# Kernel optimization log

Hardware: AMD Instinct MI355X
Metric: run time of the kernel (lower is better)

The kernel has to match this reference:

```python
import jax, jax.numpy as jnp
import numpy as np

D_STATE = 8
DT_RANK = 16
D_CONV = 4


def layernorm(x, w, b, eps=1e-5):
    mu = jnp.mean(x, axis=-1, keepdims=True)
    var = jnp.var(x, axis=-1, keepdims=True)
    return (x - mu) * jax.lax.rsqrt(var + eps) * w + b


def silu(x):
    return x * jax.nn.sigmoid(x)


def dwconv_causal(x, w, b):
    # x: [B,L,D], w: [D,K] depthwise causal conv (mamba conv1d, padding=K-1 then truncate)
    K = w.shape[1]
    xp = jnp.pad(x, ((0, 0), (K - 1, 0), (0, 0)))
    y = jax.lax.conv_general_dilated(
        xp, w.T[:, None, :], (1,), 'VALID',
        dimension_numbers=('NWC', 'WIO', 'NWC'),
        feature_group_count=w.shape[0])
    return y + b


def selective_scan(u, dt, A, Bm, Cm, Dp):
    # u, dt: [b,l,d]; A: [d,n]; Bm, Cm: [b,l,n]; Dp: [d]
    def step(h, inp):
        dt_t, B_t, C_t, u_t = inp           # [b,d],[b,n],[b,n],[b,d]
        dA = jnp.exp(dt_t[..., None] * A)   # [b,d,n]
        h = dA * h + dt_t[..., None] * B_t[:, None, :] * u_t[..., None]
        y = jnp.einsum('bdn,bn->bd', h, C_t)
        return h, y
    b, l, d = u.shape
    h0 = jnp.zeros((b, d, A.shape[1]), u.dtype)
    xs = (dt.transpose(1, 0, 2), Bm.transpose(1, 0, 2),
          Cm.transpose(1, 0, 2), u.transpose(1, 0, 2))
    _, ys = jax.lax.scan(step, h0, xs)
    return ys.transpose(1, 0, 2) + u * Dp


def scan_dir(x, xe, cw, cb, cew, ceb, xpw, dtw, dtb, A_log, Dp):
    # one scan direction: u from x (input0 path), dt/B/C from xe (extra_emb path)
    xc = silu(dwconv_causal(x, cw, cb))
    ec = silu(dwconv_causal(xe, cew, ceb))
    dbl = ec @ xpw.T                                   # [b,l,dt_rank+2n]
    dtr = dbl[..., :DT_RANK]
    Bm = dbl[..., DT_RANK:DT_RANK + D_STATE]
    Cm = dbl[..., DT_RANK + D_STATE:]
    dt = jax.nn.softplus(dtr @ dtw.T + dtb)
    A = -jnp.exp(A_log)
    return selective_scan(xc, dt, A, Bm, Cm, Dp)


def forward(input0, input1, norm0_w, norm0_b, norm1_w, norm1_b,
            in_proj_w, in_proj_extra_w,
            convx_w, convx_b, conve_w, conve_b,
            convx_w_r, convx_b_r, conve_w_r, conve_b_r,
            xproj_w, xproj_w_r, dtproj_w, dtproj_b, dtproj_w_r, dtproj_b_r,
            A_log, A_log_r, Dp, Dp_r, outnorm_w, outnorm_b, outproj_w):
    skip = input0
    h0 = layernorm(input0, norm0_w, norm0_b)
    h1 = layernorm(input1, norm1_w, norm1_b)
    xz = h0 @ in_proj_w.T                     # [b,l,2d]
    d = in_proj_w.shape[0] // 2
    x, z = xz[..., :d], xz[..., d:]
    xe = h1 @ in_proj_extra_w.T               # [b,l,d]
    # forward-direction scan
    y_f = scan_dir(x, xe, convx_w, convx_b, conve_w, conve_b,
                   xproj_w, dtproj_w, dtproj_b, A_log, Dp)
    # backward-direction scan (flip sequence, scan, flip back)
    xr, xer = jnp.flip(x, 1), jnp.flip(xe, 1)
    y_b = scan_dir(xr, xer, convx_w_r, convx_b_r, conve_w_r, conve_b_r,
                   xproj_w_r, dtproj_w_r, dtproj_b_r, A_log_r, Dp_r)
    y = (y_f + jnp.flip(y_b, 1)) * 0.5        # if_devide_out=True
    y = layernorm(y, outnorm_w, outnorm_b)    # use_norm=True
    y = y * silu(z)
    out = y @ outproj_w.T
    return out + skip


def setup_inputs() -> dict:
    key = jax.random.key(0)
    B, H, W, dim = 2, 128, 128, 256
    L, d, n, dtr, K = H * W, dim, D_STATE, DT_RANK, D_CONV
    ks = jax.random.split(key, 24)
    s = 0.02
    inp = {
        'input0': jax.random.normal(ks[0], (B, L, dim), jnp.float32),
        'input1': jax.random.normal(ks[1], (B, L, dim), jnp.float32),
        'norm0_w': jnp.ones((dim,), jnp.float32),
        'norm0_b': jnp.zeros((dim,), jnp.float32),
        'norm1_w': jnp.ones((dim,), jnp.float32),
        'norm1_b': jnp.zeros((dim,), jnp.float32),
        'in_proj_w': jax.random.normal(ks[2], (2 * d, dim), jnp.float32) * s,
        'in_proj_extra_w': jax.random.normal(ks[3], (d, dim), jnp.float32) * s,
        'convx_w': jax.random.normal(ks[4], (d, K), jnp.float32) * 0.2,
        'convx_b': jnp.zeros((d,), jnp.float32),
        'conve_w': jax.random.normal(ks[5], (d, K), jnp.float32) * 0.2,
        'conve_b': jnp.zeros((d,), jnp.float32),
        'convx_w_r': jax.random.normal(ks[6], (d, K), jnp.float32) * 0.2,
        'convx_b_r': jnp.zeros((d,), jnp.float32),
        'conve_w_r': jax.random.normal(ks[7], (d, K), jnp.float32) * 0.2,
        'conve_b_r': jnp.zeros((d,), jnp.float32),
        'xproj_w': jax.random.normal(ks[8], (dtr + 2 * n, d), jnp.float32) * s,
        'xproj_w_r': jax.random.normal(ks[9], (dtr + 2 * n, d), jnp.float32) * s,
        'dtproj_w': jax.random.normal(ks[10], (d, dtr), jnp.float32) * 0.1,
        'dtproj_b': jax.random.uniform(ks[11], (d,), jnp.float32, -4.0, -2.0),
        'dtproj_w_r': jax.random.normal(ks[12], (d, dtr), jnp.float32) * 0.1,
        'dtproj_b_r': jax.random.uniform(ks[13], (d,), jnp.float32, -4.0, -2.0),
        'A_log': jnp.tile(jnp.log(jnp.arange(1, n + 1, dtype=jnp.float32)), (d, 1)),
        'A_log_r': jnp.tile(jnp.log(jnp.arange(1, n + 1, dtype=jnp.float32)), (d, 1)),
        'Dp': jnp.ones((d,), jnp.float32),
        'Dp_r': jnp.ones((d,), jnp.float32),
        'outnorm_w': jnp.ones((d,), jnp.float32),
        'outnorm_b': jnp.zeros((d,), jnp.float32),
        'outproj_w': jax.random.normal(ks[14], (dim, d), jnp.float32) * s,
    }
    return inp


def reference(input0, input1, norm0_w, norm0_b, norm1_w, norm1_b,
              in_proj_w, in_proj_extra_w,
              convx_w, convx_b, conve_w, conve_b,
              convx_w_r, convx_b_r, conve_w_r, conve_b_r,
              xproj_w, xproj_w_r, dtproj_w, dtproj_b, dtproj_w_r, dtproj_b_r,
              A_log, A_log_r, Dp, Dp_r, outnorm_w, outnorm_b, outproj_w):
    return forward(input0, input1, norm0_w, norm0_b, norm1_w, norm1_b,
                   in_proj_w, in_proj_extra_w,
                   convx_w, convx_b, conve_w, conve_b,
                   convx_w_r, convx_b_r, conve_w_r, conve_b_r,
                   xproj_w, xproj_w_r, dtproj_w, dtproj_b, dtproj_w_r, dtproj_b_r,
                   A_log, A_log_r, Dp, Dp_r, outnorm_w, outnorm_b, outproj_w)
```

## Files before the change

### kernel.cpp

```cpp
#include <hip/hip_runtime.h>
#include <math.h>

#define L_SEQ 16384
#define DIM 256
#define NST 8
#define RNK 16
#define S_TOT 32768
#define NCH 512
#define CLH 32

typedef __attribute__((ext_vector_type(8))) short bf16x8;
typedef __attribute__((ext_vector_type(4))) float f32x4;

__device__ __forceinline__ float bf2f(unsigned short u) {
  union { unsigned int i; float f; } v; v.i = ((unsigned int)u) << 16; return v.f;
}
__device__ __forceinline__ unsigned short f2bf(float x) {
  union { float f; unsigned int i; } v; v.f = x;
  unsigned int r = v.i + 0x7fffu + ((v.i >> 16) & 1u);
  return (unsigned short)(r >> 16);
}
__device__ __forceinline__ float rcpf(float x) {
  return __builtin_amdgcn_rcpf(x);
}

__global__ __launch_bounds__(256) void wconv(
    const float* __restrict__ w0, const float* __restrict__ w1,
    const float* __restrict__ w2, unsigned short* __restrict__ out) {
  int i = blockIdx.x * 256 + threadIdx.x;
  if (i < 131072) out[i] = f2bf(w0[i]);
  else if (i < 196608) out[i] = f2bf(w1[i - 131072]);
  else out[i] = f2bf(w2[i - 196608]);
}

__global__ __launch_bounds__(256) void ln_norm(
    const float* __restrict__ in0, const float* __restrict__ in1,
    const float* __restrict__ w0, const float* __restrict__ b0,
    const float* __restrict__ w1, const float* __restrict__ b1,
    unsigned short* __restrict__ h0, unsigned short* __restrict__ h1) {
  int which = blockIdx.y;
  int row = blockIdx.x * 4 + (threadIdx.x >> 6);
  int lane = threadIdx.x & 63;
  const float* x = (which ? in1 : in0) + (size_t)row * DIM;
  const float* w = which ? w1 : w0;
  const float* b = which ? b1 : b0;
  unsigned short* h = which ? h1 : h0;
  float4 v = *(const float4*)&x[lane * 4];
  float s = v.x + v.y + v.z + v.w;
  float s2 = v.x * v.x + v.y * v.y + v.z * v.z + v.w * v.w;
  for (int off = 32; off; off >>= 1) {
    s += __shfl_xor(s, off);
    s2 += __shfl_xor(s2, off);
  }
  float mean = s * (1.0f / DIM);
  float var = s2 * (1.0f / DIM) - mean * mean;
  float rstd = rsqrtf(var + 1e-5f);
  float4 wv = *(const float4*)&w[lane * 4];
  float4 bv = *(const float4*)&b[lane * 4];
  ushort4 out;
  out.x = f2bf((v.x - mean) * rstd * wv.x + bv.x);
  out.y = f2bf((v.y - mean) * rstd * wv.y + bv.y);
  out.z = f2bf((v.z - mean) * rstd * wv.z + bv.z);
  out.w = f2bf((v.w - mean) * rstd * wv.w + bv.w);
  *(ushort4*)&h[(size_t)row * DIM + lane * 4] = out;
}

template <int BF16C, int ADDIN>
__global__ __launch_bounds__(256) void gemm64(
    const unsigned short* __restrict__ A, int lda,
    const unsigned short* __restrict__ Wb,
    void* __restrict__ Cv, const float* __restrict__ addp, int Nn) {
  __shared__ unsigned short As[64 * 256];
  __shared__ unsigned short Ws[64 * 256];
  int tid = threadIdx.x;
  int n0 = blockIdx.x * 64, m0 = blockIdx.y * 64;
  for (int i = 0; i < 8; ++i) {
    int f8 = tid + i * 256;
    int r = f8 >> 5, c8 = (f8 & 31) * 8;
    int sc = c8 ^ ((r & 7) << 3);
    *(uint4*)&As[r * 256 + sc] = *(const uint4*)&A[(size_t)(m0 + r) * lda + c8];
    *(uint4*)&Ws[r * 256 + sc] = *(const uint4*)&Wb[(size_t)(n0 + r) * 256 + c8];
  }
  __syncthreads();
  int wid = tid >> 6, lane = tid & 63;
  int wm = wid >> 1, wn = wid & 1;
  int l15 = lane & 15, lk = (lane >> 4) * 8;
  f32x4 acc[2][2] = {};
  for (int ks = 0; ks < 8; ++ks) {
    int kcol = ks * 32 + lk;
    bf16x8 af[2], bf_[2];
    for (int mf = 0; mf < 2; ++mf) {
      int row = wm * 32 + mf * 16 + l15;
      af[mf] = *(const bf16x8*)&As[row * 256 + (kcol ^ ((row & 7) << 3))];
    }
    for (int nf = 0; nf < 2; ++nf) {
      int row = wn * 32 + nf * 16 + l15;
      bf_[nf] = *(const bf16x8*)&Ws[row * 256 + (kcol ^ ((row & 7) << 3))];
    }
    for (int mf = 0; mf < 2; ++mf)
      for (int nf = 0; nf < 2; ++nf)
        acc[mf][nf] = __builtin_amdgcn_mfma_f32_16x16x32_bf16(
            af[mf], bf_[nf], acc[mf][nf], 0, 0, 0);
  }
  for (int mf = 0; mf < 2; ++mf)
    for (int nf = 0; nf < 2; ++nf) {
      int row = m0 + wm * 32 + mf * 16 + (lane >> 4) * 4;
      int col = n0 + wn * 32 + nf * 16 + l15;
      for (int v = 0; v < 4; ++v) {
        size_t off = (size_t)(row + v) * Nn + col;
        float val = acc[mf][nf][v];
        if (ADDIN) val += addp[off];
        if (BF16C) ((unsigned short*)Cv)[off] = f2bf(val);
        else       ((float*)Cv)[off] = val;
      }
    }
}

__global__ __launch_bounds__(256) void xproj_mfma(
    const unsigned short* __restrict__ xe,
    const float* __restrict__ conve_w, const float* __restrict__ conve_b,
    const float* __restrict__ conve_w_r, const float* __restrict__ conve_b_r,
    const float* __restrict__ xproj_w, const float* __restrict__ xproj_w_r,
    float* __restrict__ dbl2) {
  __shared__ unsigned short ecS[64 * 256];
  __shared__ unsigned short xwS[32 * 256];
  int chunk = blockIdx.x;
  int dir = blockIdx.y;
  int b = chunk >> 8;
  int t0 = (chunk & 255) * 64;
  int tid = threadIdx.x;
  const float* cw = dir ? conve_w_r : conve_w;
  const float* cb = dir ? conve_b_r : conve_b;
  const float* xw = dir ? xproj_w_r : xproj_w;

  for (int i = tid; i < 32 * 256; i += 256) {
    int o = i >> 8, dd = i & 255;
    xwS[o * 256 + (((dd & ~7) ^ ((o & 7) << 3)) | (dd & 7))] = f2bf(xw[i]);
  }

  {
    int c = tid;
    float w0 = cw[c * 4 + 0], w1 = cw[c * 4 + 1], w2 = cw[c * 4 + 2],
          w3 = cw[c * 4 + 3], bias = cb[c];
    size_t bL = (size_t)b * L_SEQ;
    auto loadx = [&](int t) -> float {
      if (t < 0) return 0.f;
      int src = dir ? (L_SEQ - 1 - t) : t;
      return bf2f(xe[(bL + src) * DIM + c]);
    };
    float xm3 = loadx(t0 - 3), xm2 = loadx(t0 - 2), xm1 = loadx(t0 - 1);
    const unsigned short* xp =
        &xe[(bL + (dir ? (L_SEQ - 1 - t0) : t0)) * DIM + c];
    int xstep = dir ? -DIM : DIM;
    int cbase = c & ~7, clow = c & 7;
    for (int tl = 0; tl < 64; ++tl) {
      float xin = bf2f(*xp); xp += xstep;
      float pre = w0 * xm3 + w1 * xm2 + w2 * xm1 + w3 * xin + bias;
      float u = pre * rcpf(1.f + __expf(-pre));
      xm3 = xm2; xm2 = xm1; xm1 = xin;
      ecS[tl * 256 + ((cbase ^ ((tl & 7) << 3)) | clow)] = f2bf(u);
    }
  }
  __syncthreads();

  int wid = tid >> 6, lane = tid & 63;
  int l15 = lane & 15, lk = (lane >> 4) * 8;
  f32x4 acc[2] = {};
  for (int kk = 0; kk < 8; ++kk) {
    int kcol = kk * 32 + lk;
    int row = wid * 16 + l15;
    bf16x8 af = *(const bf16x8*)&ecS[row * 256 + (kcol ^ ((row & 7) << 3))];
    for (int ni = 0; ni < 2; ++ni) {
      int o = ni * 16 + l15;
      bf16x8 bfr = *(const bf16x8*)&xwS[o * 256 + (kcol ^ ((o & 7) << 3))];
      acc[ni] = __builtin_amdgcn_mfma_f32_16x16x32_bf16(af, bfr, acc[ni], 0, 0, 0);
    }
  }
  size_t mbase = (size_t)dir * S_TOT + (size_t)chunk * 64;
  int rloc = wid * 16 + (lane >> 4) * 4;
  for (int ni = 0; ni < 2; ++ni) {
    int o = ni * 16 + l15;
    for (int v = 0; v < 4; ++v)
      dbl2[(mbase + rloc + v) * 32 + o] = acc[ni][v];
  }
}

__global__ __launch_bounds__(256) void dt_mfma(
    const float* __restrict__ dbl2,
    const float* __restrict__ dtw, const float* __restrict__ dtw_r,
    const float* __restrict__ dtb, const float* __restrict__ dtb_r,
    unsigned short* __restrict__ dt_arr) {
  __shared__ unsigned short dtwS[256 * 32];
  __shared__ unsigned short dtrS[64 * 32];
  __shared__ unsigned short outS[64 * 256];
  int m0 = blockIdx.x * 64;
  int dir = (blockIdx.x >= 512) ? 1 : 0;
  int tid = threadIdx.x;
  const float* dw = dir ? dtw_r : dtw;
  const float* db = dir ? dtb_r : dtb;
  {
    uint4 z; z.x = 0; z.y = 0; z.z = 0; z.w = 0;
    for (int i = tid; i < 1280; i += 256) {
      if (i < 1024) ((uint4*)dtwS)[i] = z;
      else          ((uint4*)dtrS)[i - 1024] = z;
    }
  }
  __syncthreads();
  for (int it = 0; it < 4; ++it) {
    int idx = tid + it * 256;
    int c = idx >> 2, k4 = idx & 3;
    float4 v = *(const float4*)&dw[c * 16 + k4 * 4];
    uint2 pk;
    pk.x = (unsigned int)f2bf(v.x) | ((unsigned int)f2bf(v.y) << 16);
    pk.y = (unsigned int)f2bf(v.z) | ((unsigned int)f2bf(v.w) << 16);
    int byte = c * 64 + (((k4 >> 1) ^ (c & 3)) << 4) + ((k4 & 1) << 3);
    *(uint2*)((char*)dtwS + byte) = pk;
  }
  {
    int r = tid >> 2, k4 = tid & 3;
    float4 v = *(const float4*)&dbl2[(size_t)(m0 + r) * 32 + k4 * 4];
    uint2 pk;
    pk.x = (unsigned int)f2bf(v.x) | ((unsigned int)f2bf(v.y) << 16);
    pk.y = (unsigned int)f2bf(v.z) | ((unsigned int)f2bf(v.w) << 16);
    int byte = r * 64 + (((k4 >> 1) ^ (r & 3)) << 4) + ((k4 & 1) << 3);
    *(uint2*)((char*)dtrS + byte) = pk;
  }
  __syncthreads();
  int wid = tid >> 6, lane = tid & 63;
  int l15 = lane & 15, lkc = lane >> 4;
  bf16x8 af[4];
  for (int mi = 0; mi < 4; ++mi) {
    int r = mi * 16 + l15;
    af[mi] = *(const bf16x8*)((char*)dtrS + r * 64 + ((lkc ^ (r & 3)) << 4));
  }
  f32x4 acc[4][4] = {};
  for (int ni = 0; ni < 4; ++ni) {
    int c = (wid * 4 + ni) * 16 + l15;
    bf16x8 bfr = *(const bf16x8*)((char*)dtwS + c * 64 + ((lkc ^ (c & 3)) << 4));
    for (int mi = 0; mi < 4; ++mi)
      acc[mi][ni] = __builtin_amdgcn_mfma_f32_16x16x32_bf16(
          af[mi], bfr, acc[mi][ni], 0, 0, 0);
  }
  for (int ni = 0; ni < 4; ++ni) {
    int c = (wid * 4 + ni) * 16 + l15;
    float bias_ = db[c];
    int cb_ = c & ~7, cl_ = c & 7;
    for (int mi = 0; mi < 4; ++mi) {
      int rb = mi * 16 + (lane >> 4) * 4;
      for (int v = 0; v < 4; ++v) {
        int r = rb + v;
        float xdt = acc[mi][ni][v] + bias_;
        float dtv = (xdt > 15.f) ? xdt : __logf(1.f + __expf(xdt));
        outS[r * 256 + ((cb_ ^ ((r & 7) << 3)) | cl_)] = f2bf(dtv);
      }
    }
  }
  __syncthreads();
  for (int it = 0; it < 8; ++it) {
    int i = tid + it * 256;
    int r = i >> 5, cg = (i & 31) * 8;
    uint4 val = *(const uint4*)&outS[r * 256 + (cg ^ ((r & 7) << 3))];
    *(uint4*)&dt_arr[(size_t)(m0 + r) * 256 + cg] = val;
  }
}

__global__ __launch_bounds__(256) void u_compute(
    const unsigned short* __restrict__ xz,
    const float* __restrict__ convx_w, const float* __restrict__ convx_b,
    const float* __restrict__ convx_w_r, const float* __restrict__ convx_b_r,
    unsigned short* __restrict__ u_arr) {
  int chunk = blockIdx.x;
  int dir = blockIdx.y;
  int b = chunk >> 9;
  int t0 = (chunk & 511) * 32;
  int c = threadIdx.x;
  const float* cw = dir ? convx_w_r : convx_w;
  const float* cb = dir ? convx_b_r : convx_b;
  float w0 = cw[c * 4 + 0], w1 = cw[c * 4 + 1], w2 = cw[c * 4 + 2],
        w3 = cw[c * 4 + 3], bias = cb[c];
  size_t dtbase = (size_t)dir * S_TOT + (size_t)b * L_SEQ;
  size_t bL = (size_t)b * L_SEQ;
  float xm3, xm2, xm1;
  {
    auto loadx = [&](int t) -> float {
      if (t < 0) return 0.f;
      int src = dir ? (L_SEQ - 1 - t) : t;
      return bf2f(xz[(bL + src) * 512 + c]);
    };
    xm3 = loadx(t0 - 3); xm2 = loadx(t0 - 2); xm1 = loadx(t0 - 1);
  }
  const unsigned short* xp = &xz[(bL + (dir ? (L_SEQ - 1 - t0) : t0)) * 512 + c];
  int xstep = dir ? -512 : 512;
  unsigned short* op = &u_arr[(dtbase + t0) * DIM + c];
  for (int tl = 0; tl < 32; ++tl) {
    float xin = bf2f(*xp); xp += xstep;
    float pre = w0 * xm3 + w1 * xm2 + w2 * xm1 + w3 * xin + bias;
    float u = pre * rcpf(1.f + __expf(-pre));
    xm3 = xm2; xm2 = xm1; xm1 = xin;
    *op = f2bf(u); op += DIM;
  }
}

#define DA8(FASTA)                                                    \
  float dA[NST];                                                      \
  if (FASTA) {                                                        \
    float e1 = __expf(-dtv);                                          \
    dA[0] = e1;                                                       \
    for (int n = 1; n < NST; ++n) dA[n] = dA[n - 1] * e1;             \
  } else {                                                            \
    for (int n = 0; n < NST; ++n) dA[n] = __expf(dtv * Ar[n]);        \
  }

template <int USE_UDT>
__global__ __launch_bounds__(256) void scan_pass1(
    const unsigned short* __restrict__ xz, const float* __restrict__ dbl2,
    const unsigned short* __restrict__ u_arr,
    const unsigned short* __restrict__ dt_arr,
    const float* __restrict__ convx_w, const float* __restrict__ convx_b,
    const float* __restrict__ convx_w_r, const float* __restrict__ convx_b_r,
    const float* __restrict__ dtproj_w, const float* __restrict__ dtproj_b,
    const float* __restrict__ dtproj_w_r, const float* __restrict__ dtproj_b_r,
    const float* __restrict__ A_log, const float* __restrict__ A_log_r,
    float* __restrict__ Pc, float* __restrict__ Qc) {
  int chunk = blockIdx.x, b = blockIdx.y, dir = blockIdx.z;
  int d = threadIdx.x;
  const float* al = dir ? A_log_r : A_log;
  float w0 = 0.f, w1 = 0.f, w2 = 0.f, w3 = 0.f, bias = 0.f, dbias = 0.f;
  float dwreg[RNK];
  if (!USE_UDT) {
    const float* cw = dir ? convx_w_r : convx_w;
    const float* cb = dir ? convx_b_r : convx_b;
    const float* dw = dir ? dtproj_w_r : dtproj_w;
    const float* dbp = dir ? dtproj_b_r : dtproj_b;
    w0 = cw[d * 4 + 0]; w1 = cw[d * 4 + 1]; w2 = cw[d * 4 + 2];
    w3 = cw[d * 4 + 3]; bias = cb[d]; dbias = dbp[d];
    for (int r = 0; r < RNK; ++r) dwreg[r] = dw[d * RNK + r];
  }
  float Ar[NST];
  bool fa = true;
  for (int n = 0; n < NST; ++n) {
    Ar[n] = -__expf(al[d * NST + n]);
    fa = fa && (fabsf(Ar[n] + (float)(n + 1)) < 1e-4f * (float)(n + 1));
  }
  bool fastA = (__ballot(fa) == ~0ULL);

  __shared__ float dblS[CLH][32];
  int t0 = chunk * CLH;
  size_t dtbase = (size_t)dir * S_TOT + (size_t)b * L_SEQ;
  if (USE_UDT) {
    int i = d;
    dblS[i >> 3][i & 7] = dbl2[(dtbase + t0 + (i >> 3)) * 32 + 16 + (i & 7)];
  } else {
    for (int i = d; i < CLH * 32; i += 256)
      dblS[i >> 5][i & 31] = dbl2[(dtbase + t0) * 32 + i];
  }
  __syncthreads();
  auto loadx = [&](int t) -> float {
    if (t < 0) return 0.f;
    int srct = dir ? (L_SEQ - 1 - t) : t;
    return bf2f(xz[((size_t)b * L_SEQ + srct) * 512 + d]);
  };
  float xm3 = 0.f, xm2 = 0.f, xm1 = 0.f;
  if (!USE_UDT) { xm3 = loadx(t0 - 3); xm2 = loadx(t0 - 2); xm1 = loadx(t0 - 1); }
  const unsigned short* up = &u_arr[(dtbase + t0) * DIM + d];
  const unsigned short* dtp = &dt_arr[(dtbase + t0) * DIM + d];
  float Q[NST];
  for (int n = 0; n < NST; ++n) Q[n] = 0.f;
  float sdt = 0.f;
  const int BOFF = USE_UDT ? 0 : 16;

#define P1_STEP(FASTA)                                                     \
  {                                                                        \
    const float* row = dblS[tl];                                           \
    float u, dtv;                                                          \
    if (USE_UDT) {                                                         \
      u = bf2f(*up); up += DIM;                                            \
      dtv = bf2f(*dtp); dtp += DIM;                                        \
    } else {                                                               \
      float xin = loadx(t0 + tl);                                          \
      float pre = w0 * xm3 + w1 * xm2 + w2 * xm1 + w3 * xin + bias;        \
      u = pre * rcpf(1.f + __expf(-pre));                                  \
      xm3 = xm2; xm2 = xm1; xm1 = xin;                                     \
      float4 q0 = *(const float4*)(row);                                   \
      float4 q1 = *(const float4*)(row + 4);                               \
      float4 q2 = *(const float4*)(row + 8);                               \
      float4 q3 = *(const float4*)(row + 12);                              \
      float xdt = dbias + q0.x * dwreg[0] + q0.y * dwreg[1] +              \
                  q0.z * dwreg[2] + q0.w * dwreg[3] + q1.x * dwreg[4] +    \
                  q1.y * dwreg[5] + q1.z * dwreg[6] + q1.w * dwreg[7] +    \
                  q2.x * dwreg[8] + q2.y * dwreg[9] + q2.z * dwreg[10] +   \
                  q2.w * dwreg[11] + q3.x * dwreg[12] + q3.y * dwreg[13] + \
                  q3.z * dwreg[14] + q3.w * dwreg[15];                     \
      dtv = (xdt > 15.f) ? xdt : __logf(1.f + __expf(xdt));                \
    }                                                                      \
    float du = dtv * u;                                                    \
    sdt += dtv;                                                            \
    DA8(FASTA)                                                             \
    float4 B0 = *(const float4*)(row + BOFF);                              \
    float4 B1 = *(const float4*)(row + BOFF + 4);                          \
    Q[0] = dA[0] * Q[0] + du * B0.x; Q[1] = dA[1] * Q[1] + du * B0.y;      \
    Q[2] = dA[2] * Q[2] + du * B0.z; Q[3] = dA[3] * Q[3] + du * B0.w;      \
    Q[4] = dA[4] * Q[4] + du * B1.x; Q[5] = dA[5] * Q[5] + du * B1.y;      \
    Q[6] = dA[6] * Q[6] + du * B1.z; Q[7] = dA[7] * Q[7] + du * B1.w;      \
  }

  if (fastA) {
    for (int tl = 0; tl < CLH; ++tl) P1_STEP(1)
  } else {
    for (int tl = 0; tl < CLH; ++tl) P1_STEP(0)
  }
#undef P1_STEP

  float P[NST];
  if (fastA) {
    float E = __expf(-sdt);
    P[0] = E;
    for (int n = 1; n < NST; ++n) P[n] = P[n - 1] * E;
  } else {
    for (int n = 0; n < NST; ++n) P[n] = __expf(Ar[n] * sdt);
  }
  size_t obase = ((((size_t)(dir * 2 + b)) * NCH + chunk) * DIM + d) * NST;
  for (int n = 0; n < NST; ++n) { Pc[obase + n] = P[n]; Qc[obase + n] = Q[n]; }
}

__global__ __launch_bounds__(256) void scan_mid(
    float* __restrict__ Pc, const float* __restrict__ Qc) {
  int idx = blockIdx.x * 256 + threadIdx.x;
  int dn = idx & 2047;
  int db_ = idx >> 11;
  size_t base = (size_t)db_ * NCH * 2048 + dn;
  float h = 0.f;
  for (int c0 = 0; c0 < NCH; c0 += 8) {
    size_t off = base + (size_t)c0 * 2048;
    float P[8], Q[8];
#pragma unroll
    for (int j = 0; j < 8; ++j) {
      P[j] = Pc[off + (size_t)j * 2048];
      Q[j] = Qc[off + (size_t)j * 2048];
    }
#pragma unroll
    for (int j = 0; j < 8; ++j) {
      Pc[off + (size_t)j * 2048] = h;
      h = P[j] * h + Q[j];
    }
  }
}

template <int MODE>
__global__ __launch_bounds__(256) void scan_pass2(
    const unsigned short* __restrict__ xz, const float* __restrict__ dbl2,
    unsigned short* __restrict__ u_arr,
    const unsigned short* __restrict__ dt_arr,
    const float* __restrict__ convx_w, const float* __restrict__ convx_b,
    const float* __restrict__ convx_w_r, const float* __restrict__ convx_b_r,
    const float* __restrict__ dtproj_w, const float* __restrict__ dtproj_b,
    const float* __restrict__ dtproj_w_r, const float* __restrict__ dtproj_b_r,
    const float* __restrict__ A_log, const float* __restrict__ A_log_r,
    const float* __restrict__ Dp, const float* __restrict__ Dp_r,
    const float* __restrict__ Hinit, unsigned short* __restrict__ ycomb,
    int dirParam) {
  int chunk = blockIdx.x, b = blockIdx.y;
  int dir = MODE ? blockIdx.z : dirParam;
  int d = threadIdx.x;
  const float* al = dir ? A_log_r : A_log;
  float Dv = (dir ? Dp_r : Dp)[d];
  float w0 = 0.f, w1 = 0.f, w2 = 0.f, w3 = 0.f, bias = 0.f, dbias = 0.f;
  float dwreg[RNK];
  if (!MODE) {
    const float* cw = dir ? convx_w_r : convx_w;
    const float* cb = dir ? convx_b_r : convx_b;
    const float* dw = dir ? dtproj_w_r : dtproj_w;
    const float* dbp = dir ? dtproj_b_r : dtproj_b;
    w0 = cw[d * 4 + 0]; w1 = cw[d * 4 + 1]; w2 = cw[d * 4 + 2];
    w3 = cw[d * 4 + 3]; bias = cb[d];
    dbias = dbp[d];
    for (int r = 0; r < RNK; ++r) dwreg[r] = dw[d * RNK + r];
  }
  float Ar[NST];
  bool fa = true;
  for (int n = 0; n < NST; ++n) {
    Ar[n] = -__expf(al[d * NST + n]);
    fa = fa && (fabsf(Ar[n] + (float)(n + 1)) < 1e-4f * (float)(n + 1));
  }
  bool fastA = (__ballot(fa) == ~0ULL);

  __shared__ float dblS[CLH][32];
  int t0 = chunk * CLH;
  size_t dtbase = (size_t)dir * S_TOT + (size_t)b * L_SEQ;
  if (MODE) {
    for (int i = d; i < CLH * 16; i += 256)
      dblS[i >> 4][i & 15] = dbl2[(dtbase + t0 + (i >> 4)) * 32 + 16 + (i & 15)];
  } else {
    for (int i = d; i < CLH * 32; i += 256)
      dblS[i >> 5][i & 31] = dbl2[(dtbase + t0) * 32 + i];
  }
  __syncthreads();
  auto loadx = [&](int t) -> float {
    if (t < 0) return 0.f;
    int srct = dir ? (L_SEQ - 1 - t) : t;
    return bf2f(xz[((size_t)b * L_SEQ + srct) * 512 + d]);
  };
  float xm3 = 0.f, xm2 = 0.f, xm1 = 0.f;
  if (!MODE) { xm3 = loadx(t0 - 3); xm2 = loadx(t0 - 2); xm1 = loadx(t0 - 1); }
  float h[NST];
  size_t hbase = ((((size_t)(dir * 2 + b)) * NCH + chunk) * DIM + d) * NST;
  for (int n = 0; n < NST; ++n) h[n] = Hinit[hbase + n];
  unsigned short* up = &u_arr[(dtbase + t0) * DIM + d];
  const unsigned short* dtp = &dt_arr[(dtbase + t0) * DIM + d];
  unsigned short* yc = &ycomb[((size_t)b * L_SEQ + t0) * DIM + d];
  const int BOFF = MODE ? 0 : 16;
  const int COFF = MODE ? 8 : 24;

#define P2_STEP(FASTA)                                                     \
  {                                                                        \
    int t = t0 + tl;                                                       \
    const float* row = dblS[tl];                                           \
    float u, dtv;                                                          \
    if (MODE) {                                                            \
      u = bf2f(*up);                                                       \
      dtv = bf2f(*dtp); dtp += DIM;                                        \
    } else {                                                               \
      float xin = loadx(t);                                                \
      float pre = w0 * xm3 + w1 * xm2 + w2 * xm1 + w3 * xin + bias;        \
      u = pre * rcpf(1.f + __expf(-pre));                                  \
      xm3 = xm2; xm2 = xm1; xm1 = xin;                                     \
      float4 q0 = *(const float4*)(row);                                   \
      float4 q1 = *(const float4*)(row + 4);                               \
      float4 q2 = *(const float4*)(row + 8);                               \
      float4 q3 = *(const float4*)(row + 12);                              \
      float xdt = dbias + q0.x * dwreg[0] + q0.y * dwreg[1] +              \
                  q0.z * dwreg[2] + q0.w * dwreg[3] + q1.x * dwreg[4] +    \
                  q1.y * dwreg[5] + q1.z * dwreg[6] + q1.w * dwreg[7] +    \
                  q2.x * dwreg[8] + q2.y * dwreg[9] + q2.z * dwreg[10] +   \
                  q2.w * dwreg[11] + q3.x * dwreg[12] + q3.y * dwreg[13] + \
                  q3.z * dwreg[14] + q3.w * dwreg[15];                     \
      dtv = (xdt > 15.f) ? xdt : __logf(1.f + __expf(xdt));                \
    }                                                                      \
    float du = dtv * u;                                                    \
    DA8(FASTA)                                                             \
    float4 B0 = *(const float4*)(row + BOFF);                              \
    float4 B1 = *(const float4*)(row + BOFF + 4);                          \
    float4 C0 = *(const float4*)(row + COFF);                              \
    float4 C1 = *(const float4*)(row + COFF + 4);                          \
    h[0] = dA[0] * h[0] + du * B0.x; h[1] = dA[1] * h[1] + du * B0.y;      \
    h[2] = dA[2] * h[2] + du * B0.z; h[3] = dA[3] * h[3] + du * B0.w;      \
    h[4] = dA[4] * h[4] + du * B1.x; h[5] = dA[5] * h[5] + du * B1.y;      \
    h[6] = dA[6] * h[6] + du * B1.z; h[7] = dA[7] * h[7] + du * B1.w;      \
    float y = C0.x * h[0] + C0.y * h[1] + C0.z * h[2] + C0.w * h[3] +      \
              C1.x * h[4] + C1.y * h[5] + C1.z * h[6] + C1.w * h[7] +      \
              u * Dv;                                                      \
    if (MODE) {                                                            \
      if (dir == 0) *yc = f2bf(y);                                         \
      else          *up = f2bf(y);                                         \
      up += DIM; yc += DIM;                                                \
    } else if (dir == 0) {                                                 \
      ycomb[((size_t)b * L_SEQ + t) * DIM + d] = f2bf(y);                  \
    } else {                                                               \
      size_t o = ((size_t)b * L_SEQ + (L_SEQ - 1 - t)) * DIM + d;          \
      float prev = bf2f(ycomb[o]);                                         \
      ycomb[o] = f2bf(0.5f * (prev + y));                                  \
    }                                                                      \
  }

  if (fastA) {
    for (int tl = 0; tl < CLH; ++tl) P2_STEP(1)
  } else {
    for (int tl = 0; tl < CLH; ++tl) P2_STEP(0)
  }
#undef P2_STEP
}

template <int MERGED>
__global__ __launch_bounds__(256) void combine_ln(
    const unsigned short* __restrict__ ycomb,
    const unsigned short* __restrict__ ybu,
    unsigned short* __restrict__ xz,
    const float* __restrict__ onw, const float* __restrict__ onb) {
  int m = blockIdx.x * 4 + (threadIdx.x >> 6);
  int lane = threadIdx.x & 63;
  ushort4 y4 = *(const ushort4*)&ycomb[(size_t)m * DIM + lane * 4];
  float v0 = bf2f(y4.x), v1 = bf2f(y4.y), v2 = bf2f(y4.z), v3 = bf2f(y4.w);
  if (MERGED) {
    int b = m >> 14, l = m & (L_SEQ - 1);
    size_t fo = ((size_t)S_TOT + (size_t)b * L_SEQ + (L_SEQ - 1 - l)) * DIM +
                lane * 4;
    ushort4 yb4 = *(const ushort4*)&ybu[fo];
    v0 = 0.5f * (v0 + bf2f(yb4.x)); v1 = 0.5f * (v1 + bf2f(yb4.y));
    v2 = 0.5f * (v2 + bf2f(yb4.z)); v3 = 0.5f * (v3 + bf2f(yb4.w));
  }
  float s = v0 + v1 + v2 + v3;
  float s2 = v0 * v0 + v1 * v1 + v2 * v2 + v3 * v3;
  for (int off = 32; off; off >>= 1) {
    s += __shfl_xor(s, off);
    s2 += __shfl_xor(s2, off);
  }
  float mean = s * (1.0f / DIM);
  float var = s2 * (1.0f / DIM) - mean * mean;
  float rstd = rsqrtf(var + 1e-5f);
  ushort4 z4 = *(const ushort4*)&xz[(size_t)m * 512 + 256 + lane * 4];
  float zf[4] = {bf2f(z4.x), bf2f(z4.y), bf2f(z4.z), bf2f(z4.w)};
  float vf[4] = {v0, v1, v2, v3};
  ushort4 out;
  unsigned short* op = (unsigned short*)&out;
  for (int j = 0; j < 4; ++j) {
    int c = lane * 4 + j;
    float ln = (vf[j] - mean) * rstd * onw[c] + onb[c];
    op[j] = f2bf(ln * (zf[j] * rcpf(1.f + __expf(-zf[j]))));
  }
  *(ushort4*)&xz[(size_t)m * 512 + lane * 4] = out;
}

extern "C" void kernel_launch(void* const* d_in, const int* in_sizes, int n_in,
                              void* d_out, int out_size, void* d_ws, size_t ws_size,
                              hipStream_t stream) {
  const float* input0 = (const float*)d_in[0];
  const float* input1 = (const float*)d_in[1];
  const float* norm0_w = (const float*)d_in[2];
  const float* norm0_b = (const float*)d_in[3];
  const float* norm1_w = (const float*)d_in[4];
  const float* norm1_b = (const float*)d_in[5];
  const float* in_proj_w = (const float*)d_in[6];
  const float* in_proj_extra_w = (const float*)d_in[7];
  const float* convx_w = (const float*)d_in[8];
  const float* convx_b = (const float*)d_in[9];
  const float* conve_w = (const float*)d_in[10];
  const float* conve_b = (const float*)d_in[11];
  const float* convx_w_r = (const float*)d_in[12];
  const float* convx_b_r = (const float*)d_in[13];
  const float* conve_w_r = (const float*)d_in[14];
  const float* conve_b_r = (const float*)d_in[15];
  const float* xproj_w = (const float*)d_in[16];
  const float* xproj_w_r = (const float*)d_in[17];
  const float* dtproj_w = (const float*)d_in[18];
  const float* dtproj_b = (const float*)d_in[19];
  const float* dtproj_w_r = (const float*)d_in[20];
  const float* dtproj_b_r = (const float*)d_in[21];
  const float* A_log = (const float*)d_in[22];
  const float* A_log_r = (const float*)d_in[23];
  const float* Dp = (const float*)d_in[24];
  const float* Dp_r = (const float*)d_in[25];
  const float* outnorm_w = (const float*)d_in[26];
  const float* outnorm_b = (const float*)d_in[27];
  const float* outproj_w = (const float*)d_in[28];

  char* w = (char*)d_ws;
  unsigned short* xz    = (unsigned short*)(w + 0);
  unsigned short* h1    = (unsigned short*)(w + 0);
  unsigned short* h0    = (unsigned short*)(w + 33554432);
  unsigned short* ycomb = (unsigned short*)(w + 33554432);
  float* Qc   = (float*)(w + 33554432);
  unsigned short* xe    = (unsigned short*)(w + 50331648);
  float* Pc   = (float*)(w + 50331648);
  float* dbl2 = (float*)(w + 67108864);
  unsigned short* wb = (unsigned short*)(w + 75497472);
  unsigned short* wb_in  = wb;
  unsigned short* wb_ex  = wb + 131072;
  unsigned short* wb_out = wb + 196608;
  unsigned short* u_arr  = (unsigned short*)(w + 76021760);
  unsigned short* dt_arr = (unsigned short*)(w + 109576192);
  const bool big = ws_size >= 76021760ULL + 67108864ULL;

  wconv<<<dim3(1024), 256, 0, stream>>>(in_proj_w, in_proj_extra_w, outproj_w, wb);
  ln_norm<<<dim3(S_TOT / 4, 2), 256, 0, stream>>>(
      input0, input1, norm0_w, norm0_b, norm1_w, norm1_b, h0, h1);
  gemm64<1, 0><<<dim3(4, 512), 256, 0, stream>>>(h1, DIM, wb_ex, xe, nullptr, 256);
  gemm64<1, 0><<<dim3(8, 512), 256, 0, stream>>>(h0, DIM, wb_in, xz, nullptr, 512);
  xproj_mfma<<<dim3(512, 2), 256, 0, stream>>>(
      xe, conve_w, conve_b, conve_w_r, conve_b_r, xproj_w, xproj_w_r, dbl2);
  if (big) {
    dt_mfma<<<dim3(1024), 256, 0, stream>>>(
        dbl2, dtproj_w, dtproj_w_r, dtproj_b, dtproj_b_r, dt_arr);
    u_compute<<<dim3(1024, 2), 256, 0, stream>>>(
        xz, convx_w, convx_b, convx_w_r, convx_b_r, u_arr);
    scan_pass1<1><<<dim3(NCH, 2, 2), 256, 0, stream>>>(
        xz, dbl2, u_arr, dt_arr, convx_w, convx_b, convx_w_r, convx_b_r,
        dtproj_w, dtproj_b, dtproj_w_r, dtproj_b_r, A_log, A_log_r, Pc, Qc);
  } else {
    scan_pass1<0><<<dim3(NCH, 2, 2), 256, 0, stream>>>(
        xz, dbl2, u_arr, dt_arr, convx_w, convx_b, convx_w_r, convx_b_r,
        dtproj_w, dtproj_b, dtproj_w_r, dtproj_b_r, A_log, A_log_r, Pc, Qc);
  }
  scan_mid<<<dim3(32), 256, 0, stream>>>(Pc, Qc);
  if (big) {
    scan_pass2<1><<<dim3(NCH, 2, 2), 256, 0, stream>>>(
        xz, dbl2, u_arr, dt_arr, convx_w, convx_b, convx_w_r, convx_b_r,
        dtproj_w, dtproj_b, dtproj_w_r, dtproj_b_r, A_log, A_log_r,
        Dp, Dp_r, Pc, ycomb, 0);
    combine_ln<1><<<dim3(S_TOT / 4), 256, 0, stream>>>(
        ycomb, u_arr, xz, outnorm_w, outnorm_b);
  } else {
    for (int dir = 0; dir < 2; ++dir)
      scan_pass2<0><<<dim3(NCH, 2), 256, 0, stream>>>(
          xz, dbl2, u_arr, dt_arr, convx_w, convx_b, convx_w_r, convx_b_r,
          dtproj_w, dtproj_b, dtproj_w_r, dtproj_b_r, A_log, A_log_r,
          Dp, Dp_r, Pc, ycomb, dir);
    combine_ln<0><<<dim3(S_TOT / 4), 256, 0, stream>>>(
        ycomb, nullptr, xz, outnorm_w, outnorm_b);
  }
  gemm64<0, 1><<<dim3(4, 512), 256, 0, stream>>>(
      xz, 512, wb_out, d_out, input0, 256);
}
```

Baseline: 237.0 us.

## Compute local scan outputs in pass1, apply carry-in correction in pass2

Pass1 now computes the chunk-local output y (with zero initial state) and the cumulative dt sum per step, and writes them over the u and dt buffers in place. Pass2 no longer reruns the recurrence. It adds the contribution of the chunk's incoming state, decayed by exp(A*cumsum dt), dotted with C. This moves the per-step state update out of pass2, leaving only a dot product and exponentials there. Pass1 gains the C loads and two stores per step. Storing the cumulative dt sum and the local y in bf16 may reduce accuracy.

```diff
diff --git a/kernel.cpp b/kernel.cpp
--- a/kernel.cpp
+++ b/kernel.cpp
@@ -314,17 +314,19 @@
 template <int USE_UDT>
 __global__ __launch_bounds__(256) void scan_pass1(
     const unsigned short* __restrict__ xz, const float* __restrict__ dbl2,
-    const unsigned short* __restrict__ u_arr,
-    const unsigned short* __restrict__ dt_arr,
+    unsigned short* __restrict__ u_arr,
+    unsigned short* __restrict__ dt_arr,
     const float* __restrict__ convx_w, const float* __restrict__ convx_b,
     const float* __restrict__ convx_w_r, const float* __restrict__ convx_b_r,
     const float* __restrict__ dtproj_w, const float* __restrict__ dtproj_b,
     const float* __restrict__ dtproj_w_r, const float* __restrict__ dtproj_b_r,
     const float* __restrict__ A_log, const float* __restrict__ A_log_r,
+    const float* __restrict__ Dp, const float* __restrict__ Dp_r,
     float* __restrict__ Pc, float* __restrict__ Qc) {
   int chunk = blockIdx.x, b = blockIdx.y, dir = blockIdx.z;
   int d = threadIdx.x;
   const float* al = dir ? A_log_r : A_log;
+  float Dv = (dir ? Dp_r : Dp)[d];
   float w0 = 0.f, w1 = 0.f, w2 = 0.f, w3 = 0.f, bias = 0.f, dbias = 0.f;
   float dwreg[RNK];
   if (!USE_UDT) {
@@ -348,8 +350,8 @@
   int t0 = chunk * CLH;
   size_t dtbase = (size_t)dir * S_TOT + (size_t)b * L_SEQ;
   if (USE_UDT) {
-    int i = d;
-    dblS[i >> 3][i & 7] = dbl2[(dtbase + t0 + (i >> 3)) * 32 + 16 + (i & 7)];
+    for (int i = d; i < CLH * 16; i += 256)
+      dblS[i >> 4][i & 15] = dbl2[(dtbase + t0 + (i >> 4)) * 32 + 16 + (i & 15)];
   } else {
     for (int i = d; i < CLH * 32; i += 256)
       dblS[i >> 5][i & 31] = dbl2[(dtbase + t0) * 32 + i];
@@ -362,20 +364,21 @@
   };
   float xm3 = 0.f, xm2 = 0.f, xm1 = 0.f;
   if (!USE_UDT) { xm3 = loadx(t0 - 3); xm2 = loadx(t0 - 2); xm1 = loadx(t0 - 1); }
-  const unsigned short* up = &u_arr[(dtbase + t0) * DIM + d];
-  const unsigned short* dtp = &dt_arr[(dtbase + t0) * DIM + d];
+  unsigned short* up = &u_arr[(dtbase + t0) * DIM + d];
+  unsigned short* dtp = &dt_arr[(dtbase + t0) * DIM + d];
   float Q[NST];
   for (int n = 0; n < NST; ++n) Q[n] = 0.f;
   float sdt = 0.f;
   const int BOFF = USE_UDT ? 0 : 16;
+  const int COFF = USE_UDT ? 8 : 24;
 
 #define P1_STEP(FASTA)                                                     \
   {                                                                        \
     const float* row = dblS[tl];                                           \
     float u, dtv;                                                          \
     if (USE_UDT) {                                                         \
-      u = bf2f(*up); up += DIM;                                            \
-      dtv = bf2f(*dtp); dtp += DIM;                                        \
+      u = bf2f(*up);                                                       \
+      dtv = bf2f(*dtp);                                                    \
     } else {                                                               \
       float xin = loadx(t0 + tl);                                          \
       float pre = w0 * xm3 + w1 * xm2 + w2 * xm1 + w3 * xin + bias;        \
@@ -402,6 +405,15 @@
     Q[2] = dA[2] * Q[2] + du * B0.z; Q[3] = dA[3] * Q[3] + du * B0.w;      \
     Q[4] = dA[4] * Q[4] + du * B1.x; Q[5] = dA[5] * Q[5] + du * B1.y;      \
     Q[6] = dA[6] * Q[6] + du * B1.z; Q[7] = dA[7] * Q[7] + du * B1.w;      \
+    if (USE_UDT) {                                                         \
+      float4 C0 = *(const float4*)(row + COFF);                            \
+      float4 C1 = *(const float4*)(row + COFF + 4);                        \
+      float yl = C0.x * Q[0] + C0.y * Q[1] + C0.z * Q[2] + C0.w * Q[3] +   \
+                 C1.x * Q[4] + C1.y * Q[5] + C1.z * Q[6] + C1.w * Q[7] +   \
+                 u * Dv;                                                   \
+      *up = f2bf(yl); up += DIM;                                           \
+      *dtp = f2bf(sdt); dtp += DIM;                                        \
+    }                                                                      \
   }
 
   if (fastA) {
@@ -488,8 +500,8 @@
   int t0 = chunk * CLH;
   size_t dtbase = (size_t)dir * S_TOT + (size_t)b * L_SEQ;
   if (MODE) {
-    for (int i = d; i < CLH * 16; i += 256)
-      dblS[i >> 4][i & 15] = dbl2[(dtbase + t0 + (i >> 4)) * 32 + 16 + (i & 15)];
+    int i = d;
+    dblS[i >> 3][i & 7] = dbl2[(dtbase + t0 + (i >> 3)) * 32 + 24 + (i & 7)];
   } else {
     for (int i = d; i < CLH * 32; i += 256)
       dblS[i >> 5][i & 31] = dbl2[(dtbase + t0) * 32 + i];
@@ -508,18 +520,32 @@
   unsigned short* up = &u_arr[(dtbase + t0) * DIM + d];
   const unsigned short* dtp = &dt_arr[(dtbase + t0) * DIM + d];
   unsigned short* yc = &ycomb[((size_t)b * L_SEQ + t0) * DIM + d];
-  const int BOFF = MODE ? 0 : 16;
-  const int COFF = MODE ? 8 : 24;
+
+  if (MODE) {
+    for (int tl = 0; tl < CLH; ++tl) {
+      float yl = bf2f(*up);
+      float dtv = bf2f(*dtp); dtp += DIM;
+      DA8(fastA)
+      const float* row = dblS[tl];
+      float4 C0 = *(const float4*)(row);
+      float4 C1 = *(const float4*)(row + 4);
+      float y = yl + C0.x * dA[0] * h[0] + C0.y * dA[1] * h[1] +
+                C0.z * dA[2] * h[2] + C0.w * dA[3] * h[3] +
+                C1.x * dA[4] * h[4] + C1.y * dA[5] * h[5] +
+                C1.z * dA[6] * h[6] + C1.w * dA[7] * h[7];
+      if (dir == 0) *yc = f2bf(y);
+      else          *up = f2bf(y);
+      up += DIM; yc += DIM;
+    }
+    return;
+  }
 
 #define P2_STEP(FASTA)                                                     \
   {                                                                        \
     int t = t0 + tl;                                                       \
     const float* row = dblS[tl];                                           \
     float u, dtv;                                                          \
-    if (MODE) {                                                            \
-      u = bf2f(*up);                                                       \
-      dtv = bf2f(*dtp); dtp += DIM;                                        \
-    } else {                                                               \
+    {                                                                      \
       float xin = loadx(t);                                                \
       float pre = w0 * xm3 + w1 * xm2 + w2 * xm1 + w3 * xin + bias;        \
       u = pre * rcpf(1.f + __expf(-pre));                                  \
@@ -538,10 +564,10 @@
     }                                                                      \
     float du = dtv * u;                                                    \
     DA8(FASTA)                                                             \
-    float4 B0 = *(const float4*)(row + BOFF);                              \
-    float4 B1 = *(const float4*)(row + BOFF + 4);                          \
-    float4 C0 = *(const float4*)(row + COFF);                              \
-    float4 C1 = *(const float4*)(row + COFF + 4);                          \
+    float4 B0 = *(const float4*)(row + 16);                                \
+    float4 B1 = *(const float4*)(row + 20);                                \
+    float4 C0 = *(const float4*)(row + 24);                                \
+    float4 C1 = *(const float4*)(row + 28);                                \
     h[0] = dA[0] * h[0] + du * B0.x; h[1] = dA[1] * h[1] + du * B0.y;      \
     h[2] = dA[2] * h[2] + du * B0.z; h[3] = dA[3] * h[3] + du * B0.w;      \
     h[4] = dA[4] * h[4] + du * B1.x; h[5] = dA[5] * h[5] + du * B1.y;      \
@@ -549,11 +575,7 @@
     float y = C0.x * h[0] + C0.y * h[1] + C0.z * h[2] + C0.w * h[3] +      \
               C1.x * h[4] + C1.y * h[5] + C1.z * h[6] + C1.w * h[7] +      \
               u * Dv;                                                      \
-    if (MODE) {                                                            \
-      if (dir == 0) *yc = f2bf(y);                                         \
-      else          *up = f2bf(y);                                         \
-      up += DIM; yc += DIM;                                                \
-    } else if (dir == 0) {                                                 \
+    if (dir == 0) {                                                        \
       ycomb[((size_t)b * L_SEQ + t) * DIM + d] = f2bf(y);                  \
     } else {                                                               \
       size_t o = ((size_t)b * L_SEQ + (L_SEQ - 1 - t)) * DIM + d;          \
@@ -674,11 +696,13 @@
         xz, convx_w, convx_b, convx_w_r, convx_b_r, u_arr);
     scan_pass1<1><<<dim3(NCH, 2, 2), 256, 0, stream>>>(
         xz, dbl2, u_arr, dt_arr, convx_w, convx_b, convx_w_r, convx_b_r,
-        dtproj_w, dtproj_b, dtproj_w_r, dtproj_b_r, A_log, A_log_r, Pc, Qc);
+        dtproj_w, dtproj_b, dtproj_w_r, dtproj_b_r, A_log, A_log_r,
+        Dp, Dp_r, Pc, Qc);
   } else {
     scan_pass1<0><<<dim3(NCH, 2, 2), 256, 0, stream>>>(
         xz, dbl2, u_arr, dt_arr, convx_w, convx_b, convx_w_r, convx_b_r,
-        dtproj_w, dtproj_b, dtproj_w_r, dtproj_b_r, A_log, A_log_r, Pc, Qc);
+        dtproj_w, dtproj_b, dtproj_w_r, dtproj_b_r, A_log, A_log_r,
+        Dp, Dp_r, Pc, Qc);
   }
   scan_mid<<<dim3(32), 256, 0, stream>>>(Pc, Qc);
   if (big) {
```

Measured after the change: 265.8 us. 1.12x slower.
